# Optimization experiments

Measured on AMD Instinct MI355X. Metric: run time of the kernel, lower is better.

Reference implementation:

```python
import jax, jax.numpy as jnp
import numpy as np

DIM = 1024
N_HEADS = 16
HEAD_DIM = DIM // N_HEADS
B, T = 2, 2048


def setup_inputs() -> dict:
    key = jax.random.key(0)
    ks = jax.random.split(key, 5)
    s = 0.02
    return {
        "x": jax.random.normal(ks[0], (B, T, DIM), dtype=jnp.float32),
        "w_qkv": jax.random.normal(ks[1], (DIM, 3 * DIM), dtype=jnp.float32) * s,
        "b_qkv": jnp.zeros((3 * DIM,), dtype=jnp.float32),
        "w_proj": jax.random.normal(ks[2], (DIM, DIM), dtype=jnp.float32) * s,
        "b_proj": jnp.zeros((DIM,), dtype=jnp.float32),
    }


def reference(x, w_qkv, b_qkv, w_proj, b_proj):
    Bb, Tt, C = x.shape
    H, Dh = N_HEADS, HEAD_DIM
    qkv = x @ w_qkv + b_qkv                       # [B,T,3C]
    qkv = qkv.reshape(Bb, Tt, 3, H, Dh)
    q = jnp.transpose(qkv[:, :, 0], (0, 2, 1, 3))  # [B,H,T,Dh]
    k = jnp.transpose(qkv[:, :, 1], (0, 2, 1, 3))
    v = jnp.transpose(qkv[:, :, 2], (0, 2, 1, 3))
    att = jnp.einsum("bhqd,bhkd->bhqk", q, k) / jnp.sqrt(jnp.float32(Dh))
    causal = jnp.tril(jnp.ones((Tt, Tt), dtype=bool))
    att = jnp.where(causal[None, None], att, -jnp.inf)
    att = jax.nn.softmax(att, axis=-1)
    out = jnp.einsum("bhqk,bhkd->bhqd", att, v)    # [B,H,T,Dh]
    out = jnp.transpose(out, (0, 2, 1, 3)).reshape(Bb, Tt, C)
    return out @ w_proj + b_proj
```

## Files before the change

kernel.cpp:

```cpp
#include <hip/hip_runtime.h>
#include <math.h>

#define DIMC 1024
#define NH 16
#define HD 64
#define BATCH 2
#define SEQ 2048
#define M_ROWS (BATCH * SEQ)
#define QKV_N (3 * DIMC)

typedef __attribute__((ext_vector_type(8))) short bf16x8;
typedef __attribute__((ext_vector_type(4))) float f32x4;
typedef __attribute__((ext_vector_type(2))) unsigned int u32x2;

static __device__ __forceinline__ unsigned short f2bf(float f) {
    union { float f; unsigned u; } v; v.f = f;
    unsigned r = v.u + 0x7fffu + ((v.u >> 16) & 1u);
    return (unsigned short)(r >> 16);
}

static __device__ __forceinline__ unsigned cvt_pk_bf16(float lo, float hi) {
    unsigned r;
    asm("v_cvt_pk_bf16_f32 %0, %1, %2" : "=v"(r) : "v"(lo), "v"(hi));
    return r;
}

#define GLOAD16(g, l)                                                          \
    __builtin_amdgcn_global_load_lds(                                          \
        (__attribute__((address_space(1))) void*)(void*)(g),                   \
        (__attribute__((address_space(3))) void*)(void*)(l), 16, 0, 0)

__global__ __launch_bounds__(256) void cvt_bf16(const float* __restrict__ in,
                                                short* __restrict__ out)
{
    int i = blockIdx.x * 256 + threadIdx.x;
    float4 v = reinterpret_cast<const float4*>(in)[i];
    ushort4 o = {f2bf(v.x), f2bf(v.y), f2bf(v.z), f2bf(v.w)};
    reinterpret_cast<ushort4*>(out)[i] = o;
}

__global__ __launch_bounds__(256) void transpose_both(const float* __restrict__ wq,
                                                      short* __restrict__ wqt,
                                                      const float* __restrict__ wp,
                                                      short* __restrict__ wpt)
{
    __shared__ short tile[64][65];
    const int tid = threadIdx.x;
    const bool isq = blockIdx.x < 48;
    const int bx  = isq ? blockIdx.x : blockIdx.x - 48;
    const int C   = isq ? QKV_N : DIMC;
    const float* in = isq ? wq : wp;
    short* out      = isq ? wqt : wpt;
    const int R = DIMC;
    const int r0 = blockIdx.y * 64, c0 = bx * 64;
    #pragma unroll
    for (int i = 0; i < 4; ++i) {
        int r = i * 16 + (tid >> 4);
        int c = (tid & 15) * 4;
        float4 v = *reinterpret_cast<const float4*>(&in[(size_t)(r0 + r) * C + c0 + c]);
        tile[c + 0][r] = f2bf(v.x);
        tile[c + 1][r] = f2bf(v.y);
        tile[c + 2][r] = f2bf(v.z);
        tile[c + 3][r] = f2bf(v.w);
    }
    __syncthreads();
    #pragma unroll
    for (int i = 0; i < 4; ++i) {
        int c = i * 16 + (tid >> 4);
        int r = (tid & 15) * 4;
        ushort4 o;
        o.x = tile[c][r + 0]; o.y = tile[c][r + 1];
        o.z = tile[c][r + 2]; o.w = tile[c][r + 3];
        *reinterpret_cast<ushort4*>(&out[(size_t)(c0 + c) * R + r0 + r]) = o;
    }
}

template<int EPI>
__global__ __launch_bounds__(256) void gemm_mfma(const short* __restrict__ A,
                                                 const short* __restrict__ Bt,
                                                 const float* __restrict__ bias,
                                                 float* __restrict__ C,
                                                 short* __restrict__ Qb,
                                                 short* __restrict__ Kb,
                                                 short* __restrict__ Vt,
                                                 int M, int N, int K)
{
    __shared__ short As[2][128 * 32];
    __shared__ short Bs[2][128 * 32];

    const int tid  = threadIdx.x;
    const int wave = tid >> 6;
    const int lane = tid & 63;
    const int l16  = lane & 15;
    const int lg   = lane >> 4;
    const int wr   = wave >> 1;
    const int wc   = wave & 1;

    const int nx   = gridDim.x;
    const int flat = blockIdx.y * nx + blockIdx.x;
    const int nwg  = nx * gridDim.y;
    const int q8   = nwg >> 3;
    const int nf   = (flat & 7) * q8 + (flat >> 3);
    const int by   = nf & 31;
    const int bx   = nf >> 5;

    const int brow = by * 128;
    const int bcol = bx * 128;

    const short* ga = A  + (size_t)brow * K;
    const short* gb = Bt + (size_t)bcol * K;

    f32x4 acc[4][4] = {};

    for (int k0 = 0; k0 < K; k0 += 64) {
        __syncthreads();
        #pragma unroll
        for (int li = 0; li < 4; ++li) {
            int c   = li * 256 + tid;
            int ks  = c >> 9;
            int row = (c & 511) >> 2;
            int sub = c & 3;
            size_t goff = (size_t)row * K + k0 + ks * 32 + sub * 8;
            GLOAD16(ga + goff, &As[0][0] + c * 8);
            GLOAD16(gb + goff, &Bs[0][0] + c * 8);
        }
        __syncthreads();

        #pragma unroll
        for (int ks = 0; ks < 2; ++ks) {
            bf16x8 af[4], bf[4];
            #pragma unroll
            for (int m = 0; m < 4; ++m)
                af[m] = *reinterpret_cast<const bf16x8*>(
                    &As[ks][(wr * 64 + m * 16 + l16) * 32 + lg * 8]);
            #pragma unroll
            for (int n = 0; n < 4; ++n)
                bf[n] = *reinterpret_cast<const bf16x8*>(
                    &Bs[ks][(wc * 64 + n * 16 + l16) * 32 + lg * 8]);
            #pragma unroll
            for (int m = 0; m < 4; ++m)
                #pragma unroll
                for (int n = 0; n < 4; ++n)
                    acc[m][n] = __builtin_amdgcn_mfma_f32_16x16x32_bf16(
                        af[m], bf[n], acc[m][n], 0, 0, 0);
        }
    }

    if (EPI == 0) {
        #pragma unroll
        for (int m = 0; m < 4; ++m) {
            #pragma unroll
            for (int n = 0; n < 4; ++n) {
                int col = bcol + wc * 64 + n * 16 + l16;
                float bv = bias[col];
                #pragma unroll
                for (int r = 0; r < 4; ++r) {
                    int row = brow + wr * 64 + m * 16 + lg * 4 + r;
                    C[(size_t)row * N + col] = acc[m][n][r] + bv;
                }
            }
        }
    } else {
        const int sec = bcol >> 10;
        #pragma unroll
        for (int m = 0; m < 4; ++m) {
            const int t0 = brow + wr * 64 + m * 16 + lg * 4;
            const int bb = t0 >> 11;
            const int tl = t0 & 2047;
            #pragma unroll
            for (int n = 0; n < 4; ++n) {
                int col = bcol + wc * 64 + n * 16 + l16;
                int hh  = (col & 1023) >> 6;
                int d   = col & 63;
                float bv = bias[col];
                if (sec == 0) {
                    #pragma unroll
                    for (int r = 0; r < 4; ++r)
                        Qb[((size_t)(bb * NH + hh) * SEQ + tl + r) * HD + d] =
                            (short)f2bf((acc[m][n][r] + bv) * 0.18033688011112042f);
                } else if (sec == 1) {
                    #pragma unroll
                    for (int r = 0; r < 4; ++r)
                        Kb[((size_t)(bb * NH + hh) * SEQ + tl + r) * HD + d] =
                            (short)f2bf(acc[m][n][r] + bv);
                } else {
                    ushort4 o;
                    o.x = f2bf(acc[m][n][0] + bv);
                    o.y = f2bf(acc[m][n][1] + bv);
                    o.z = f2bf(acc[m][n][2] + bv);
                    o.w = f2bf(acc[m][n][3] + bv);
                    *reinterpret_cast<ushort4*>(
                        &Vt[((size_t)(bb * NH + hh) * HD + d) * SEQ + tl]) = o;
                }
            }
        }
    }
}

static __device__ __forceinline__ void attn_step_sw(const bf16x8 qf[2],
                                                    f32x4 acc[4],
                                                    float& lsum,
                                                    const char* kshc, const char* vshc,
                                                    char* pw,
                                                    int l16, int lg,
                                                    bool do_mask, int qloc)
{
    const f32x4 fzero = {0.f, 0.f, 0.f, 0.f};
    f32x4 sa[4];
    __builtin_amdgcn_s_setprio(1);
    #pragma unroll
    for (int kc = 0; kc < 4; ++kc) {
        sa[kc] = fzero;
        int row = kc * 16 + l16;
        #pragma unroll
        for (int c = 0; c < 2; ++c) {
            int byte = (row << 7) + (c << 6) + (lg << 4);
            byte ^= ((row & 7) << 4);
            bf16x8 kf = *reinterpret_cast<const bf16x8*>(kshc + byte);
            sa[kc] = __builtin_amdgcn_mfma_f32_16x16x32_bf16(kf, qf[c], sa[kc], 0, 0, 0);
        }
    }
    __builtin_amdgcn_s_setprio(0);

    #pragma unroll
    for (int kc = 0; kc < 4; ++kc) {
        const int kl = kc * 16 + lg * 4;
        float p0, p1, p2, p3;
        {
            float s0 = sa[kc][0], s1 = sa[kc][1], s2 = sa[kc][2], s3 = sa[kc][3];
            if (do_mask) {
                if (kl + 0 > qloc) s0 = -1e30f;
                if (kl + 1 > qloc) s1 = -1e30f;
                if (kl + 2 > qloc) s2 = -1e30f;
                if (kl + 3 > qloc) s3 = -1e30f;
            }
            p0 = exp2f(s0); p1 = exp2f(s1); p2 = exp2f(s2); p3 = exp2f(s3);
        }
        lsum += (p0 + p1) + (p2 + p3);
        u32x2 pk;
        pk.x = cvt_pk_bf16(p0, p1);
        pk.y = cvt_pk_bf16(p2, p3);
        int byte = (l16 << 7) + (kc << 5) + (lg << 3);
        byte ^= ((l16 & 7) << 4);
        *reinterpret_cast<u32x2*>(pw + byte) = pk;
    }

    __builtin_amdgcn_s_setprio(1);
    #pragma unroll
    for (int c = 0; c < 2; ++c) {
        int pbyte = (l16 << 7) + (c << 6) + (lg << 4);
        pbyte ^= ((l16 & 7) << 4);
        bf16x8 pf = *reinterpret_cast<const bf16x8*>(pw + pbyte);
        #pragma unroll
        for (int dg = 0; dg < 4; ++dg) {
            int vrow  = dg * 16 + l16;
            int vbyte = (vrow << 7) + (c << 6) + (lg << 4);
            vbyte ^= ((vrow & 7) << 4);
            bf16x8 vf = *reinterpret_cast<const bf16x8*>(vshc + vbyte);
            acc[dg] = __builtin_amdgcn_mfma_f32_16x16x32_bf16(pf, vf, acc[dg], 0, 0, 0);
        }
    }
    __builtin_amdgcn_s_setprio(0);
}

__global__ __launch_bounds__(128) void attn_mfma(const short* __restrict__ Qb,
                                                 const short* __restrict__ Kb,
                                                 const short* __restrict__ Vt,
                                                 short* __restrict__ out)
{
    const int tid  = threadIdx.x;
    const int wave = tid >> 6;
    const int lane = tid & 63;
    const int l16  = lane & 15;
    const int lg   = lane >> 4;

    const int raw = blockIdx.x;
    const int wg  = (raw & 7) * 128 + (raw >> 3);
    const int i = wg & 31;
    const int h = (wg >> 5) & 15;
    const int b = wg >> 9;

    const int qtA = i;
    const int qtB = 63 - i;
    const int ktA = i >> 1;
    const int ktB = (63 - i) >> 1;
    const int wro = wave * 16;

    __shared__ short ksh[64 * 64];
    __shared__ short vsh[64 * 64];
    __shared__ short psh[2][16 * 64];

    const short* qgb = Qb + (size_t)(b * NH + h) * SEQ * HD;
    bf16x8 qfA[2], qfB[2];
    {
        const short* qa = qgb + (size_t)(qtA * 32 + wro + l16) * HD;
        qfA[0] = *reinterpret_cast<const bf16x8*>(qa + 8 * lg);
        qfA[1] = *reinterpret_cast<const bf16x8*>(qa + 32 + 8 * lg);
        const short* qb = qgb + (size_t)(qtB * 32 + wro + l16) * HD;
        qfB[0] = *reinterpret_cast<const bf16x8*>(qb + 8 * lg);
        qfB[1] = *reinterpret_cast<const bf16x8*>(qb + 32 + 8 * lg);
    }

    const short* kgb = Kb + (size_t)(b * NH + h) * SEQ * HD;
    const short* vgb = Vt + (size_t)(b * NH + h) * HD * SEQ;

    const int row0 = tid >> 3;
    const int col0 = (tid & 7) * 8;

    bf16x8 kreg[4], vreg[4];
    #pragma unroll
    for (int it = 0; it < 4; ++it) {
        int row = row0 + it * 16;
        kreg[it] = *reinterpret_cast<const bf16x8*>(kgb + (size_t)row * HD + col0);
        vreg[it] = *reinterpret_cast<const bf16x8*>(vgb + (size_t)row * SEQ + col0);
    }

    f32x4 accA[4] = {}, accB[4] = {};
    float lsumA = 0.f, lsumB = 0.f;

    const int qlocA = (qtA & 1) * 32 + wro + l16;
    const int qlocB = (qtB & 1) * 32 + wro + l16;
    char* pw = (char*)psh[wave];
    const char* kshc = (const char*)ksh;
    const char* vshc = (const char*)vsh;

    for (int kt = 0; kt <= ktB; ++kt) {
        __syncthreads();
        #pragma unroll
        for (int it = 0; it < 4; ++it) {
            int row  = row0 + it * 16;
            int byte = (row << 7) + (col0 << 1);
            byte ^= ((row & 7) << 4);
            *reinterpret_cast<bf16x8*>((char*)ksh + byte) = kreg[it];
            *reinterpret_cast<bf16x8*>((char*)vsh + byte) = vreg[it];
        }
        if (kt < ktB) {
            #pragma unroll
            for (int it = 0; it < 4; ++it) {
                int row = row0 + it * 16;
                kreg[it] = *reinterpret_cast<const bf16x8*>(
                    kgb + (size_t)((kt + 1) * 64 + row) * HD + col0);
                vreg[it] = *reinterpret_cast<const bf16x8*>(
                    vgb + (size_t)row * SEQ + (kt + 1) * 64 + col0);
            }
        }
        __syncthreads();

        attn_step_sw(qfB, accB, lsumB, kshc, vshc, pw,
                     l16, lg, kt == ktB, qlocB);
        if (kt <= ktA)
            attn_step_sw(qfA, accA, lsumA, kshc, vshc, pw,
                         l16, lg, kt == ktA, qlocA);
    }

    lsumA += __shfl_xor(lsumA, 16);
    lsumA += __shfl_xor(lsumA, 32);
    lsumB += __shfl_xor(lsumB, 16);
    lsumB += __shfl_xor(lsumB, 32);
    const float linvA = 1.0f / lsumA;
    const float linvB = 1.0f / lsumB;

    #pragma unroll
    for (int r = 0; r < 4; ++r) {
        float invA = __shfl(linvA, lg * 4 + r);
        float invB = __shfl(linvB, lg * 4 + r);
        int qa = qtA * 32 + wro + lg * 4 + r;
        int qb = qtB * 32 + wro + lg * 4 + r;
        short* opa = out + ((size_t)(b * SEQ + qa)) * DIMC + h * HD;
        short* opb = out + ((size_t)(b * SEQ + qb)) * DIMC + h * HD;
        #pragma unroll
        for (int dg = 0; dg < 4; ++dg) {
            opa[dg * 16 + l16] = (short)f2bf(accA[dg][r] * invA);
            opb[dg * 16 + l16] = (short)f2bf(accB[dg][r] * invB);
        }
    }
}

extern "C" void kernel_launch(void* const* d_in, const int* in_sizes, int n_in,
                              void* d_out, int out_size, void* d_ws, size_t ws_size,
                              hipStream_t stream)
{
    const float* x      = (const float*)d_in[0];
    const float* w_qkv  = (const float*)d_in[1];
    const float* b_qkv  = (const float*)d_in[2];
    const float* w_proj = (const float*)d_in[3];
    const float* b_proj = (const float*)d_in[4];
    float* out = (float*)d_out;

    short* Qb   = (short*)d_ws;
    short* Kb   = Qb + (size_t)M_ROWS * DIMC;
    short* Vt   = Kb + (size_t)M_ROWS * DIMC;
    short* attn = Vt + (size_t)M_ROWS * DIMC;
    short* xb   = attn + (size_t)M_ROWS * DIMC;
    short* Wqt  = xb + (size_t)M_ROWS * DIMC;
    short* Wpt  = Wqt + (size_t)DIMC * QKV_N;

    cvt_bf16<<<dim3(M_ROWS * DIMC / 4 / 256), dim3(256), 0, stream>>>(x, xb);
    transpose_both<<<dim3(64, 16), dim3(256), 0, stream>>>(w_qkv, Wqt, w_proj, Wpt);

    gemm_mfma<1><<<dim3(QKV_N / 128, M_ROWS / 128), dim3(256), 0, stream>>>(
        xb, Wqt, b_qkv, nullptr, Qb, Kb, Vt, M_ROWS, QKV_N, DIMC);

    attn_mfma<<<dim3(BATCH * NH * 32), dim3(128), 0, stream>>>(Qb, Kb, Vt, attn);

    gemm_mfma<0><<<dim3(DIMC / 128, M_ROWS / 128), dim3(256), 0, stream>>>(
        attn, Wpt, b_proj, out, nullptr, nullptr, nullptr, M_ROWS, DIMC, DIMC);
}
```

Baseline: 118.8 us.

## Widen attention blocks to four waves with per-wave 16-row query tiles

The attention kernel now launches 256 threads (4 waves) per block instead of 128. Each wave owns its own pair of 16-row query tiles, paired from opposite ends of the causal range, and the waves share each 64-key K/V tile staged in LDS. This doubles the number of query rows that reuse each K/V tile load per block and halves the per-thread global-load work. Because each wave's two tiles end at different key tiles, waves inside a block now carry uneven work, and the per-block LDS footprint and register pressure change.

```diff
diff --git a/kernel.cpp b/kernel.cpp
--- a/kernel.cpp
+++ b/kernel.cpp
@@ -263,10 +263,10 @@
     __builtin_amdgcn_s_setprio(0);
 }
 
-__global__ __launch_bounds__(128) void attn_mfma(const short* __restrict__ Qb,
-                                                 const short* __restrict__ Kb,
-                                                 const short* __restrict__ Vt,
-                                                 short* __restrict__ out)
+__global__ void attn_mfma(const short* __restrict__ Qb,
+                          const short* __restrict__ Kb,
+                          const short* __restrict__ Vt,
+                          short* __restrict__ out)
 {
     const int tid  = threadIdx.x;
     const int wave = tid >> 6;
@@ -280,25 +280,30 @@
     const int h = (wg >> 5) & 15;
     const int b = wg >> 9;
 
-    const int qtA = i;
-    const int qtB = 63 - i;
-    const int ktA = i >> 1;
-    const int ktB = (63 - i) >> 1;
-    const int wro = wave * 16;
+    const int t1 = 4 * i + wave;
+    const int t2 = 127 - t1;
+    const int kt1 = i;
+    const int kt2 = 31 - i;
+
+    const bool t2long = (kt2 >= kt1);
+    const int tM  = t2long ? t2 : t1;
+    const int tS  = t2long ? t1 : t2;
+    const int ktM = t2long ? kt2 : kt1;
+    const int ktS = t2long ? kt1 : kt2;
 
     __shared__ short ksh[64 * 64];
     __shared__ short vsh[64 * 64];
-    __shared__ short psh[2][16 * 64];
+    __shared__ short psh[4][16 * 64];
 
     const short* qgb = Qb + (size_t)(b * NH + h) * SEQ * HD;
-    bf16x8 qfA[2], qfB[2];
+    bf16x8 qfM[2], qfS[2];
     {
-        const short* qa = qgb + (size_t)(qtA * 32 + wro + l16) * HD;
-        qfA[0] = *reinterpret_cast<const bf16x8*>(qa + 8 * lg);
-        qfA[1] = *reinterpret_cast<const bf16x8*>(qa + 32 + 8 * lg);
-        const short* qb = qgb + (size_t)(qtB * 32 + wro + l16) * HD;
-        qfB[0] = *reinterpret_cast<const bf16x8*>(qb + 8 * lg);
-        qfB[1] = *reinterpret_cast<const bf16x8*>(qb + 32 + 8 * lg);
+        const short* qm = qgb + (size_t)(tM * 16 + l16) * HD;
+        qfM[0] = *reinterpret_cast<const bf16x8*>(qm + 8 * lg);
+        qfM[1] = *reinterpret_cast<const bf16x8*>(qm + 32 + 8 * lg);
+        const short* qs = qgb + (size_t)(tS * 16 + l16) * HD;
+        qfS[0] = *reinterpret_cast<const bf16x8*>(qs + 8 * lg);
+        qfS[1] = *reinterpret_cast<const bf16x8*>(qs + 32 + 8 * lg);
     }
 
     const short* kgb = Kb + (size_t)(b * NH + h) * SEQ * HD;
@@ -307,37 +312,37 @@
     const int row0 = tid >> 3;
     const int col0 = (tid & 7) * 8;
 
-    bf16x8 kreg[4], vreg[4];
-    #pragma unroll
-    for (int it = 0; it < 4; ++it) {
-        int row = row0 + it * 16;
+    bf16x8 kreg[2], vreg[2];
+    #pragma unroll
+    for (int it = 0; it < 2; ++it) {
+        int row = row0 + it * 32;
         kreg[it] = *reinterpret_cast<const bf16x8*>(kgb + (size_t)row * HD + col0);
         vreg[it] = *reinterpret_cast<const bf16x8*>(vgb + (size_t)row * SEQ + col0);
     }
 
-    f32x4 accA[4] = {}, accB[4] = {};
-    float lsumA = 0.f, lsumB = 0.f;
-
-    const int qlocA = (qtA & 1) * 32 + wro + l16;
-    const int qlocB = (qtB & 1) * 32 + wro + l16;
+    f32x4 accM[4] = {}, accS[4] = {};
+    float lsumM = 0.f, lsumS = 0.f;
+
+    const int qlocM = (tM & 3) * 16 + l16;
+    const int qlocS = (tS & 3) * 16 + l16;
     char* pw = (char*)psh[wave];
     const char* kshc = (const char*)ksh;
     const char* vshc = (const char*)vsh;
 
-    for (int kt = 0; kt <= ktB; ++kt) {
+    for (int kt = 0; kt <= ktM; ++kt) {
         __syncthreads();
         #pragma unroll
-        for (int it = 0; it < 4; ++it) {
-            int row  = row0 + it * 16;
+        for (int it = 0; it < 2; ++it) {
+            int row  = row0 + it * 32;
             int byte = (row << 7) + (col0 << 1);
             byte ^= ((row & 7) << 4);
             *reinterpret_cast<bf16x8*>((char*)ksh + byte) = kreg[it];
             *reinterpret_cast<bf16x8*>((char*)vsh + byte) = vreg[it];
         }
-        if (kt < ktB) {
-            #pragma unroll
-            for (int it = 0; it < 4; ++it) {
-                int row = row0 + it * 16;
+        if (kt < ktM) {
+            #pragma unroll
+            for (int it = 0; it < 2; ++it) {
+                int row = row0 + it * 32;
                 kreg[it] = *reinterpret_cast<const bf16x8*>(
                     kgb + (size_t)((kt + 1) * 64 + row) * HD + col0);
                 vreg[it] = *reinterpret_cast<const bf16x8*>(
@@ -346,32 +351,32 @@
         }
         __syncthreads();
 
-        attn_step_sw(qfB, accB, lsumB, kshc, vshc, pw,
-                     l16, lg, kt == ktB, qlocB);
-        if (kt <= ktA)
-            attn_step_sw(qfA, accA, lsumA, kshc, vshc, pw,
-                         l16, lg, kt == ktA, qlocA);
-    }
-
-    lsumA += __shfl_xor(lsumA, 16);
-    lsumA += __shfl_xor(lsumA, 32);
-    lsumB += __shfl_xor(lsumB, 16);
-    lsumB += __shfl_xor(lsumB, 32);
-    const float linvA = 1.0f / lsumA;
-    const float linvB = 1.0f / lsumB;
+        attn_step_sw(qfM, accM, lsumM, kshc, vshc, pw,
+                     l16, lg, kt == ktM, qlocM);
+        if (kt <= ktS)
+            attn_step_sw(qfS, accS, lsumS, kshc, vshc, pw,
+                         l16, lg, kt == ktS, qlocS);
+    }
+
+    lsumM += __shfl_xor(lsumM, 16);
+    lsumM += __shfl_xor(lsumM, 32);
+    lsumS += __shfl_xor(lsumS, 16);
+    lsumS += __shfl_xor(lsumS, 32);
+    const float linvM = 1.0f / lsumM;
+    const float linvS = 1.0f / lsumS;
 
     #pragma unroll
     for (int r = 0; r < 4; ++r) {
-        float invA = __shfl(linvA, lg * 4 + r);
-        float invB = __shfl(linvB, lg * 4 + r);
-        int qa = qtA * 32 + wro + lg * 4 + r;
-        int qb = qtB * 32 + wro + lg * 4 + r;
-        short* opa = out + ((size_t)(b * SEQ + qa)) * DIMC + h * HD;
-        short* opb = out + ((size_t)(b * SEQ + qb)) * DIMC + h * HD;
+        float invM = __shfl(linvM, lg * 4 + r);
+        float invS = __shfl(linvS, lg * 4 + r);
+        int qm = tM * 16 + lg * 4 + r;
+        int qs = tS * 16 + lg * 4 + r;
+        short* opm = out + ((size_t)(b * SEQ + qm)) * DIMC + h * HD;
+        short* ops = out + ((size_t)(b * SEQ + qs)) * DIMC + h * HD;
         #pragma unroll
         for (int dg = 0; dg < 4; ++dg) {
-            opa[dg * 16 + l16] = (short)f2bf(accA[dg][r] * invA);
-            opb[dg * 16 + l16] = (short)f2bf(accB[dg][r] * invB);
+            opm[dg * 16 + l16] = (short)f2bf(accM[dg][r] * invM);
+            ops[dg * 16 + l16] = (short)f2bf(accS[dg][r] * invS);
         }
     }
 }
@@ -401,7 +406,7 @@
     gemm_mfma<1><<<dim3(QKV_N / 128, M_ROWS / 128), dim3(256), 0, stream>>>(
         xb, Wqt, b_qkv, nullptr, Qb, Kb, Vt, M_ROWS, QKV_N, DIMC);
 
-    attn_mfma<<<dim3(BATCH * NH * 32), dim3(128), 0, stream>>>(Qb, Kb, Vt, attn);
+    attn_mfma<<<dim3(BATCH * NH * 32), dim3(256), 0, stream>>>(Qb, Kb, Vt, attn);
 
     gemm_mfma<0><<<dim3(DIMC / 128, M_ROWS / 128), dim3(256), 0, stream>>>(
         attn, Wpt, b_proj, out, nullptr, nullptr, nullptr, M_ROWS, DIMC, DIMC);
```

Result: slower. 142.5 us (+19.9%).

## Widen attention workgroups to four waves sharing 128-key K/V tiles

Applied to the files above, without the earlier changes.

The attention kernel now uses 256-thread workgroups in which two wave pairs handle adjacent query-tile pairs and share a 128-key K/V tile staged in LDS as two 64-key halves. The grid is halved, so each K/V tile fetched from global memory serves twice as many query rows, and the number of barriers per key processed drops. In exchange, LDS use per block doubles, fewer blocks are launched (512 instead of 1024), and the pair of waves with the shorter causal range may sit idle on the last tiles.

```diff
diff --git a/kernel.cpp b/kernel.cpp
--- a/kernel.cpp
+++ b/kernel.cpp
@@ -263,10 +263,10 @@
     __builtin_amdgcn_s_setprio(0);
 }
 
-__global__ __launch_bounds__(128) void attn_mfma(const short* __restrict__ Qb,
-                                                 const short* __restrict__ Kb,
-                                                 const short* __restrict__ Vt,
-                                                 short* __restrict__ out)
+__global__ __launch_bounds__(256, 2) void attn_mfma(const short* __restrict__ Qb,
+                                                    const short* __restrict__ Kb,
+                                                    const short* __restrict__ Vt,
+                                                    short* __restrict__ out)
 {
     const int tid  = threadIdx.x;
     const int wave = tid >> 6;
@@ -275,20 +275,22 @@
     const int lg   = lane >> 4;
 
     const int raw = blockIdx.x;
-    const int wg  = (raw & 7) * 128 + (raw >> 3);
-    const int i = wg & 31;
-    const int h = (wg >> 5) & 15;
-    const int b = wg >> 9;
-
-    const int qtA = i;
-    const int qtB = 63 - i;
-    const int ktA = i >> 1;
-    const int ktB = (63 - i) >> 1;
-    const int wro = wave * 16;
-
-    __shared__ short ksh[64 * 64];
-    __shared__ short vsh[64 * 64];
-    __shared__ short psh[2][16 * 64];
+    const int wg  = (raw & 7) * 64 + (raw >> 3);
+    const int i = wg & 15;
+    const int h = (wg >> 4) & 15;
+    const int b = wg >> 8;
+
+    const int wp  = wave >> 1;
+    const int wro = (wave & 1) * 16;
+    const int qtA = 2 * i + wp;
+    const int qtB = 63 - 2 * i - wp;
+    const int ktA = i;
+    const int ktB = 31 - i;
+    const int ktB128 = ktB >> 1;
+
+    __shared__ short ksh[2][64 * 64];
+    __shared__ short vsh[2][64 * 64];
+    __shared__ short psh[4][16 * 64];
 
     const short* qgb = Qb + (size_t)(b * NH + h) * SEQ * HD;
     bf16x8 qfA[2], qfB[2];
@@ -310,9 +312,12 @@
     bf16x8 kreg[4], vreg[4];
     #pragma unroll
     for (int it = 0; it < 4; ++it) {
-        int row = row0 + it * 16;
-        kreg[it] = *reinterpret_cast<const bf16x8*>(kgb + (size_t)row * HD + col0);
-        vreg[it] = *reinterpret_cast<const bf16x8*>(vgb + (size_t)row * SEQ + col0);
+        int half = it >> 1;
+        int row  = row0 + (it & 1) * 32;
+        kreg[it] = *reinterpret_cast<const bf16x8*>(
+            kgb + (size_t)(half * 64 + row) * HD + col0);
+        vreg[it] = *reinterpret_cast<const bf16x8*>(
+            vgb + (size_t)row * SEQ + half * 64 + col0);
     }
 
     f32x4 accA[4] = {}, accB[4] = {};
@@ -321,36 +326,43 @@
     const int qlocA = (qtA & 1) * 32 + wro + l16;
     const int qlocB = (qtB & 1) * 32 + wro + l16;
     char* pw = (char*)psh[wave];
-    const char* kshc = (const char*)ksh;
-    const char* vshc = (const char*)vsh;
-
-    for (int kt = 0; kt <= ktB; ++kt) {
+
+    for (int kt = 0; kt <= ktB128; ++kt) {
         __syncthreads();
         #pragma unroll
         for (int it = 0; it < 4; ++it) {
-            int row  = row0 + it * 16;
+            int half = it >> 1;
+            int row  = row0 + (it & 1) * 32;
             int byte = (row << 7) + (col0 << 1);
             byte ^= ((row & 7) << 4);
-            *reinterpret_cast<bf16x8*>((char*)ksh + byte) = kreg[it];
-            *reinterpret_cast<bf16x8*>((char*)vsh + byte) = vreg[it];
-        }
-        if (kt < ktB) {
+            *reinterpret_cast<bf16x8*>((char*)ksh[half] + byte) = kreg[it];
+            *reinterpret_cast<bf16x8*>((char*)vsh[half] + byte) = vreg[it];
+        }
+        if (kt < ktB128) {
             #pragma unroll
             for (int it = 0; it < 4; ++it) {
-                int row = row0 + it * 16;
+                int half = it >> 1;
+                int row  = row0 + (it & 1) * 32;
                 kreg[it] = *reinterpret_cast<const bf16x8*>(
-                    kgb + (size_t)((kt + 1) * 64 + row) * HD + col0);
+                    kgb + (size_t)((kt + 1) * 128 + half * 64 + row) * HD + col0);
                 vreg[it] = *reinterpret_cast<const bf16x8*>(
-                    vgb + (size_t)row * SEQ + (kt + 1) * 64 + col0);
+                    vgb + (size_t)row * SEQ + (kt + 1) * 128 + half * 64 + col0);
             }
         }
         __syncthreads();
 
-        attn_step_sw(qfB, accB, lsumB, kshc, vshc, pw,
-                     l16, lg, kt == ktB, qlocB);
-        if (kt <= ktA)
-            attn_step_sw(qfA, accA, lsumA, kshc, vshc, pw,
-                         l16, lg, kt == ktA, qlocA);
+        #pragma unroll
+        for (int s = 0; s < 2; ++s) {
+            const int k64 = 2 * kt + s;
+            if (k64 <= ktB)
+                attn_step_sw(qfB, accB, lsumB,
+                             (const char*)ksh[s], (const char*)vsh[s], pw,
+                             l16, lg, k64 == ktB, qlocB);
+            if (k64 <= ktA)
+                attn_step_sw(qfA, accA, lsumA,
+                             (const char*)ksh[s], (const char*)vsh[s], pw,
+                             l16, lg, k64 == ktA, qlocA);
+        }
     }
 
     lsumA += __shfl_xor(lsumA, 16);
@@ -401,7 +413,7 @@
     gemm_mfma<1><<<dim3(QKV_N / 128, M_ROWS / 128), dim3(256), 0, stream>>>(
         xb, Wqt, b_qkv, nullptr, Qb, Kb, Vt, M_ROWS, QKV_N, DIMC);
 
-    attn_mfma<<<dim3(BATCH * NH * 32), dim3(128), 0, stream>>>(Qb, Kb, Vt, attn);
+    attn_mfma<<<dim3(BATCH * NH * 16), dim3(256), 0, stream>>>(Qb, Kb, Vt, attn);
 
     gemm_mfma<0><<<dim3(DIMC / 128, M_ROWS / 128), dim3(256), 0, stream>>>(
         attn, Wpt, b_proj, out, nullptr, nullptr, nullptr, M_ROWS, DIMC, DIMC);
```

Measured after the change: 115.1 us. 3.1% less time.
